# Optimization experiments

Measured on AMD Instinct MI355X. Metric: run time of the kernel, lower is better.

The kernel has to match this reference:

```python
import jax, jax.numpy as jnp
import numpy as np

N = 100000   # nodes
E = 800000   # edges (avg degree 8)
D = 128      # input_dim == output_dim
H = 4        # num_heads
DH = D // H  # head_dim = 32


def setup_inputs() -> dict:
    key = jax.random.key(0)
    ks = jax.random.split(key, 12)
    s = 1.0 / np.sqrt(D)
    x = jax.random.normal(ks[0], (N, D), jnp.float32)
    row = jnp.sort(jax.random.randint(ks[1], (E,), 0, N))  # destination (query) nodes
    col = jax.random.randint(ks[2], (E,), 0, N)            # source (key/value) nodes
    Wq = jax.random.normal(ks[3], (D, D), jnp.float32) * s
    bq = jax.random.normal(ks[4], (D,), jnp.float32) * 0.01
    Wk = jax.random.normal(ks[5], (D, D), jnp.float32) * s
    bk = jax.random.normal(ks[6], (D,), jnp.float32) * 0.01
    Wv = jax.random.normal(ks[7], (D, D), jnp.float32) * s
    bv = jax.random.normal(ks[8], (D,), jnp.float32) * 0.01
    Wo = jax.random.normal(ks[9], (D, D), jnp.float32) * s
    bo = jax.random.normal(ks[10], (D,), jnp.float32) * 0.01
    return {"x": x, "row": row, "col": col, "Wq": Wq, "bq": bq, "Wk": Wk,
            "bk": bk, "Wv": Wv, "bv": bv, "Wo": Wo, "bo": bo}


def reference(x, row, col, Wq, bq, Wk, bk, Wv, bv, Wo, bo):
    n = x.shape[0]
    # projections; reshape (N, head_dim, num_heads) exactly as the torch code
    # NOTE: source scales q by k.size(-1)**0.5 == sqrt(num_heads) (quirk, kept faithful)
    scale = jnp.asarray(H, x.dtype) ** 0.5
    q = ((x @ Wq.T + bq).reshape(n, DH, H)) / scale
    k = (x @ Wk.T + bk).reshape(n, DH, H)
    v = (x @ Wv.T + bv).reshape(n, DH, H)
    # bsddmm: per-edge, per-head scores s[e,h] = q[row[e],:,h] . k[col[e],:,h]
    s = jnp.einsum('edh,edh->eh', q[row], k[col])  # (E, H)
    # sparse row-wise softmax over incoming edges of each destination node
    m = jax.ops.segment_max(s, row, num_segments=n)      # (N, H)
    e = jnp.exp(s - m[row])                               # (E, H)
    z = jax.ops.segment_sum(e, row, num_segments=n)      # (N, H)
    a = e / z[row]                                        # (E, H) attention weights
    # bspmm: y[i,:,h] = sum_{e: row[e]=i} a[e,h] * v[col[e],:,h]
    y = jax.ops.segment_sum(a[:, None, :] * v[col], row, num_segments=n)  # (N, DH, H)
    return y.reshape(n, D) @ Wo.T + bo
```

## Files before the change

kernel.cpp:

```cpp
#include <hip/hip_runtime.h>
#include <hip/hip_bf16.h>
#include <hip/hip_fp16.h>
#include <math.h>

#define D 128
#define H 4

typedef __attribute__((ext_vector_type(8))) short bf16x8;
typedef __attribute__((ext_vector_type(4))) float f32x4;

__device__ __forceinline__ unsigned short f32_to_bf16_rne(float f) {
    union { float f; unsigned u; } c; c.f = f;
    unsigned u = c.u;
    return (unsigned short)((u + 0x7FFFu + ((u >> 16) & 1u)) >> 16);
}
__device__ __forceinline__ float bf16_to_f32(unsigned short h) {
    union { unsigned u; float f; } c; c.u = ((unsigned)h) << 16;
    return c.f;
}

__global__ __launch_bounds__(256) void convert_split(
    const float* __restrict__ in, unsigned short* __restrict__ hi,
    unsigned short* __restrict__ lo, int n4)
{
    int i = blockIdx.x * blockDim.x + threadIdx.x;
    if (i >= n4) return;
    float4 v = ((const float4*)in)[i];
    ushort4 h, l;
    h.x = f32_to_bf16_rne(v.x); l.x = f32_to_bf16_rne(v.x - bf16_to_f32(h.x));
    h.y = f32_to_bf16_rne(v.y); l.y = f32_to_bf16_rne(v.y - bf16_to_f32(h.y));
    h.z = f32_to_bf16_rne(v.z); l.z = f32_to_bf16_rne(v.z - bf16_to_f32(h.z));
    h.w = f32_to_bf16_rne(v.w); l.w = f32_to_bf16_rne(v.w - bf16_to_f32(h.w));
    ((ushort4*)hi)[i] = h;
    ((ushort4*)lo)[i] = l;
}

__global__ __launch_bounds__(256) void convert_w(
    const float* __restrict__ Wq, const float* __restrict__ Wk,
    const float* __restrict__ Wv, const float* __restrict__ Wo,
    unsigned short* __restrict__ wh, unsigned short* __restrict__ wl)
{
    int i = blockIdx.x * blockDim.x + threadIdx.x;
    if (i >= D * D) return;
    int r = i >> 7;
    int c = i & 127;
    int pr = ((r & 3) << 5) | (r >> 2);
    int pc = ((c & 3) << 5) | (c >> 2);
    const float* Ws[4] = {Wq, Wk, Wv, Wo};
#pragma unroll
    for (int m = 0; m < 4; ++m) {
        float f = Ws[m][i];
        unsigned short h = f32_to_bf16_rne(f);
        unsigned short l = f32_to_bf16_rne(f - bf16_to_f32(h));
        int dst = (m < 3) ? (pr * D + c) : (r * D + pc);
        wh[m * D * D + dst] = h;
        wl[m * D * D + dst] = l;
    }
}

#define RT 64

__global__ __launch_bounds__(512) void gemm_tile(
    const unsigned short* __restrict__ xh, const unsigned short* __restrict__ xl,
    const unsigned short* __restrict__ whAll, const unsigned short* __restrict__ wlAll,
    const float* __restrict__ b0, const float* __restrict__ b1,
    const float* __restrict__ b2,
    void* __restrict__ o0, void* __restrict__ o1, void* __restrict__ o2,
    float scale0, int n, int wbase, int halfmask, int permBias)
{
    __shared__ unsigned short Ah[RT * 128];
    __shared__ unsigned short Al[RT * 128];

    const int sel = blockIdx.y;
    const unsigned short* wh = whAll + (size_t)(wbase + sel) * D * D;
    const unsigned short* wl = wlAll + (size_t)(wbase + sel) * D * D;
    const float* bias = (sel == 0) ? b0 : (sel == 1 ? b1 : b2);
    void* out        = (sel == 0) ? o0 : (sel == 1 ? o1 : o2);
    const float scale = (sel == 0) ? scale0 : 1.0f;
    const bool halfOut = (halfmask >> sel) & 1;

    const int wid  = threadIdx.x >> 6;
    const int lane = threadIdx.x & 63;
    const int quad = lane >> 4;
    const int l16  = lane & 15;
    const int m0   = blockIdx.x * RT;

    const unsigned short* wrh = wh + (size_t)(wid * 16 + l16) * D + quad * 8;
    const unsigned short* wrl = wl + (size_t)(wid * 16 + l16) * D + quad * 8;
    bf16x8 bh[4], bl[4];
#pragma unroll
    for (int kc = 0; kc < 4; ++kc) {
        bh[kc] = *(const bf16x8*)(wrh + kc * 32);
        bl[kc] = *(const bf16x8*)(wrl + kc * 32);
    }

    for (int idx = threadIdx.x; idx < RT * 16; idx += 512) {
        int r  = idx >> 4;
        int c8 = idx & 15;
        int rg = m0 + r; if (rg > n - 1) rg = n - 1;
        int cs = ((c8 ^ (r & 15)) * 8);
        *(bf16x8*)&Ah[r * 128 + cs] = *(const bf16x8*)(xh + (size_t)rg * D + c8 * 8);
        *(bf16x8*)&Al[r * 128 + cs] = *(const bf16x8*)(xl + (size_t)rg * D + c8 * 8);
    }
    __syncthreads();

    f32x4 acc[4];
#pragma unroll
    for (int rt = 0; rt < 4; ++rt) acc[rt] = (f32x4){0.f, 0.f, 0.f, 0.f};

#pragma unroll
    for (int kc = 0; kc < 4; ++kc) {
        const int cs = ((quad + 4 * kc) ^ l16) * 8;
        bf16x8 ah[4], al[4];
#pragma unroll
        for (int rt = 0; rt < 4; ++rt) {
            const int r = rt * 16 + l16;
            ah[rt] = *(const bf16x8*)&Ah[r * 128 + cs];
            al[rt] = *(const bf16x8*)&Al[r * 128 + cs];
        }
#pragma unroll
        for (int rt = 0; rt < 4; ++rt)
            acc[rt] = __builtin_amdgcn_mfma_f32_16x16x32_bf16(ah[rt], bh[kc], acc[rt], 0, 0, 0);
#pragma unroll
        for (int rt = 0; rt < 4; ++rt)
            acc[rt] = __builtin_amdgcn_mfma_f32_16x16x32_bf16(al[rt], bh[kc], acc[rt], 0, 0, 0);
#pragma unroll
        for (int rt = 0; rt < 4; ++rt)
            acc[rt] = __builtin_amdgcn_mfma_f32_16x16x32_bf16(ah[rt], bl[kc], acc[rt], 0, 0, 0);
    }

    const int colg = wid * 16 + l16;
    const int bidx = permBias ? (((colg & 31) << 2) | (colg >> 5)) : colg;
    const float bv = bias[bidx];
    if (halfOut) {
        __half* oph = (__half*)out;
#pragma unroll
        for (int rt = 0; rt < 4; ++rt) {
#pragma unroll
            for (int r = 0; r < 4; ++r) {
                int rowg = m0 + rt * 16 + quad * 4 + r;
                if (rowg < n)
                    oph[(size_t)rowg * D + colg] = __float2half(acc[rt][r] + bv);
            }
        }
    } else {
        float* opf = (float*)out;
#pragma unroll
        for (int rt = 0; rt < 4; ++rt) {
#pragma unroll
            for (int r = 0; r < 4; ++r) {
                int rowg = m0 + rt * 16 + quad * 4 + r;
                if (rowg < n)
                    opf[(size_t)rowg * D + colg] = (acc[rt][r] + bv) * scale;
            }
        }
    }
}

__global__ void build_row_start(const int* __restrict__ row,
                                int* __restrict__ row_start, int n, int e)
{
    int i = blockIdx.x * blockDim.x + threadIdx.x;
    if (i > n) return;
    int lo = 0, hi = e;
    while (lo < hi) {
        int mid = (lo + hi) >> 1;
        if (row[mid] < i) lo = mid + 1; else hi = mid;
    }
    row_start[i] = lo;
}

#define MAXDEG 64
#define WPB 4

template<bool BIG>
__device__ __forceinline__ void edge_loop(
    int lane, int sub, int grp, int deg, int e0,
    const int* cmrow, const int* __restrict__ col,
    const float4 qa, const float4 qb,
    const __half* __restrict__ k, const __half* __restrict__ v,
    float& acc0, float& acc1, float& z)
{
    for (int e = 0; e < deg; e += 4) {
        const int ei = e + grp;
        int c0, c1, c2, c3, cs;
        if (!BIG) {
            const int4 cc = *(const int4*)&cmrow[e];
            c0 = cc.x; c1 = cc.y; c2 = cc.z; c3 = cc.w;
            cs = cmrow[ei < deg ? ei : deg - 1];
        } else {
            int es = ei < deg ? ei : deg - 1;
            cs = col[e0 + es];
            int e1 = e + 1 < deg ? e + 1 : deg - 1;
            int e2 = e + 2 < deg ? e + 2 : deg - 1;
            int e3 = e + 3 < deg ? e + 3 : deg - 1;
            c0 = col[e0 + e];
            c1 = col[e0 + e1];
            c2 = col[e0 + e2];
            c3 = col[e0 + e3];
        }
        __half2 v0 = ((const __half2*)(v + ((size_t)c0 << 7)))[lane];
        __half2 v1 = ((const __half2*)(v + ((size_t)c1 << 7)))[lane];
        __half2 v2 = ((const __half2*)(v + ((size_t)c2 << 7)))[lane];
        __half2 v3 = ((const __half2*)(v + ((size_t)c3 << 7)))[lane];
        union { bf16x8 v8; __half hx[8]; } ku;
        ku.v8 = *(const bf16x8*)(k + ((size_t)cs << 7) + sub * 8);
        float p = qa.x * __half2float(ku.hx[0]) + qa.y * __half2float(ku.hx[1])
                + qa.z * __half2float(ku.hx[2]) + qa.w * __half2float(ku.hx[3])
                + qb.x * __half2float(ku.hx[4]) + qb.y * __half2float(ku.hx[5])
                + qb.z * __half2float(ku.hx[6]) + qb.w * __half2float(ku.hx[7]);
        p += __shfl_xor(p, 1);
        p += __shfl_xor(p, 2);
        float ep = (ei < deg) ? __expf(p) : 0.f;
        float a0 = __shfl(ep,      4 * grp);
        float a1 = __shfl(ep, 16 + 4 * grp);
        float a2 = __shfl(ep, 32 + 4 * grp);
        float a3 = __shfl(ep, 48 + 4 * grp);
        z += (a0 + a1) + (a2 + a3);
        acc0 += a0 * __half2float(v0.x) + a1 * __half2float(v1.x)
              + a2 * __half2float(v2.x) + a3 * __half2float(v3.x);
        acc1 += a0 * __half2float(v0.y) + a1 * __half2float(v1.y)
              + a2 * __half2float(v2.y) + a3 * __half2float(v3.y);
    }
}

__global__ __launch_bounds__(WPB * 64) void edge_attn(
    const int* __restrict__ row_start,
    const float* __restrict__ q, const __half* __restrict__ k,
    const __half* __restrict__ v, const int* __restrict__ col,
    unsigned short* __restrict__ yh, unsigned short* __restrict__ yl, int n)
{
    __shared__ int cm[WPB][MAXDEG];

    const int wid  = threadIdx.x >> 6;
    const int lane = threadIdx.x & 63;
    const int node = blockIdx.x * WPB + wid;
    if (node >= n) return;

    const int e0  = row_start[node];
    const int deg = row_start[node + 1] - e0;
    const int sub = lane & 15;
    const int grp = lane >> 4;

    const float4* q4 = (const float4*)(q + (size_t)node * D) + sub * 2;
    const float4 qa = q4[0], qb = q4[1];

    float acc0 = 0.f, acc1 = 0.f, z = 0.f;

    if (deg <= MAXDEG) {
        const int dl4 = (deg + 3) & ~3;
        for (int i = lane; i < dl4; i += 64) {
            int ii = i < deg ? i : deg - 1;
            cm[wid][i] = col[e0 + ii];
        }
        edge_loop<false>(lane, sub, grp, deg, e0, cm[wid], col, qa, qb, k, v,
                         acc0, acc1, z);
    } else {
        edge_loop<true>(lane, sub, grp, deg, e0, cm[wid], col, qa, qb, k, v,
                        acc0, acc1, z);
    }

    const float rz = (z > 0.f) ? 1.f / z : 0.f;
    acc0 *= rz;
    acc1 *= rz;

    unsigned short h0 = f32_to_bf16_rne(acc0);
    unsigned short h1 = f32_to_bf16_rne(acc1);
    ushort2 hi2, lo2;
    hi2.x = h0; hi2.y = h1;
    lo2.x = f32_to_bf16_rne(acc0 - bf16_to_f32(h0));
    lo2.y = f32_to_bf16_rne(acc1 - bf16_to_f32(h1));
    ((ushort2*)yh)[(size_t)node * 64 + lane] = hi2;
    ((ushort2*)yl)[(size_t)node * 64 + lane] = lo2;
}

extern "C" void kernel_launch(void* const* d_in, const int* in_sizes, int n_in,
                              void* d_out, int out_size, void* d_ws, size_t ws_size,
                              hipStream_t stream)
{
    const float* x   = (const float*)d_in[0];
    const int*   row = (const int*)  d_in[1];
    const int*   col = (const int*)  d_in[2];
    const float* Wq  = (const float*)d_in[3];
    const float* bq  = (const float*)d_in[4];
    const float* Wk  = (const float*)d_in[5];
    const float* bk  = (const float*)d_in[6];
    const float* Wv  = (const float*)d_in[7];
    const float* bv  = (const float*)d_in[8];
    const float* Wo  = (const float*)d_in[9];
    const float* bo  = (const float*)d_in[10];
    float* out = (float*)d_out;

    const int n = in_sizes[0] / D;
    const int e = in_sizes[1];
    const size_t ND = (size_t)n * D;

    float* ws = (float*)d_ws;
    float*  q  = ws;
    __half* kh = (__half*)(ws + ND);
    __half* vh = kh + ND;
    unsigned short* xh = (unsigned short*)(ws + 2 * ND);
    unsigned short* xl = xh + ND;
    unsigned short* yh = xh;
    unsigned short* yl = xl;
    unsigned short* wh = (unsigned short*)(ws + 3 * ND);
    unsigned short* wl = wh + 4 * D * D;
    int* row_start = (int*)(wl + 4 * D * D);

    const int n4 = (int)(ND / 4);
    const int gx = (n + RT - 1) / RT;

    convert_w<<<(D * D + 255) / 256, 256, 0, stream>>>(Wq, Wk, Wv, Wo, wh, wl);
    convert_split<<<(n4 + 255) / 256, 256, 0, stream>>>(x, xh, xl, n4);

    gemm_tile<<<dim3(gx, 3), 512, 0, stream>>>(
        xh, xl, wh, wl, bq, bk, bv,
        (void*)q, (void*)kh, (void*)vh, 0.5f, n, 0, 6, 1);

    build_row_start<<<(n + 1 + 255) / 256, 256, 0, stream>>>(row, row_start, n, e);

    edge_attn<<<(n + WPB - 1) / WPB, WPB * 64, 0, stream>>>(
        row_start, q, kh, vh, col, yh, yl, n);

    gemm_tile<<<dim3(gx, 1), 512, 0, stream>>>(
        yh, yl, wh, wl, bo, bo, bo,
        (void*)out, (void*)out, (void*)out, 1.0f, n, 3, 0, 0);
}
```

Baseline: 293.2 us.

## Fuse fp32-to-bf16 split into GEMM and loop over Q/K/V in one block

Removes the separate convert_split kernel and has the GEMM read fp32 activations directly, splitting them into bf16 hi/lo in shared memory. The QKV GEMM now loads the x tile once and loops over the three weight matrices inside a block, instead of launching a 3-wide grid that re-reads x for each. edge_attn writes fp32 y, which the output GEMM converts on load. This saves an extra kernel launch and an intermediate hi/lo round trip through memory, but the grid has a third as many blocks and each block runs the three projections serially.

Result: slower. 308.1 us (+5.1%).

```diff
diff --git a/kernel.cpp b/kernel.cpp
--- a/kernel.cpp
+++ b/kernel.cpp
@@ -17,22 +17,6 @@
 __device__ __forceinline__ float bf16_to_f32(unsigned short h) {
     union { unsigned u; float f; } c; c.u = ((unsigned)h) << 16;
     return c.f;
-}
-
-__global__ __launch_bounds__(256) void convert_split(
-    const float* __restrict__ in, unsigned short* __restrict__ hi,
-    unsigned short* __restrict__ lo, int n4)
-{
-    int i = blockIdx.x * blockDim.x + threadIdx.x;
-    if (i >= n4) return;
-    float4 v = ((const float4*)in)[i];
-    ushort4 h, l;
-    h.x = f32_to_bf16_rne(v.x); l.x = f32_to_bf16_rne(v.x - bf16_to_f32(h.x));
-    h.y = f32_to_bf16_rne(v.y); l.y = f32_to_bf16_rne(v.y - bf16_to_f32(h.y));
-    h.z = f32_to_bf16_rne(v.z); l.z = f32_to_bf16_rne(v.z - bf16_to_f32(h.z));
-    h.w = f32_to_bf16_rne(v.w); l.w = f32_to_bf16_rne(v.w - bf16_to_f32(h.w));
-    ((ushort4*)hi)[i] = h;
-    ((ushort4*)lo)[i] = l;
 }
 
 __global__ __launch_bounds__(256) void convert_w(
@@ -60,8 +44,9 @@
 
 #define RT 64
 
-__global__ __launch_bounds__(512) void gemm_tile(
-    const unsigned short* __restrict__ xh, const unsigned short* __restrict__ xl,
+template<int NSEL>
+__global__ __launch_bounds__(512) void gemm_fused(
+    const float* __restrict__ A,
     const unsigned short* __restrict__ whAll, const unsigned short* __restrict__ wlAll,
     const float* __restrict__ b0, const float* __restrict__ b1,
     const float* __restrict__ b2,
@@ -71,87 +56,99 @@
     __shared__ unsigned short Ah[RT * 128];
     __shared__ unsigned short Al[RT * 128];
 
-    const int sel = blockIdx.y;
-    const unsigned short* wh = whAll + (size_t)(wbase + sel) * D * D;
-    const unsigned short* wl = wlAll + (size_t)(wbase + sel) * D * D;
-    const float* bias = (sel == 0) ? b0 : (sel == 1 ? b1 : b2);
-    void* out        = (sel == 0) ? o0 : (sel == 1 ? o1 : o2);
-    const float scale = (sel == 0) ? scale0 : 1.0f;
-    const bool halfOut = (halfmask >> sel) & 1;
-
     const int wid  = threadIdx.x >> 6;
     const int lane = threadIdx.x & 63;
     const int quad = lane >> 4;
     const int l16  = lane & 15;
     const int m0   = blockIdx.x * RT;
 
-    const unsigned short* wrh = wh + (size_t)(wid * 16 + l16) * D + quad * 8;
-    const unsigned short* wrl = wl + (size_t)(wid * 16 + l16) * D + quad * 8;
-    bf16x8 bh[4], bl[4];
-#pragma unroll
-    for (int kc = 0; kc < 4; ++kc) {
-        bh[kc] = *(const bf16x8*)(wrh + kc * 32);
-        bl[kc] = *(const bf16x8*)(wrl + kc * 32);
-    }
-
     for (int idx = threadIdx.x; idx < RT * 16; idx += 512) {
         int r  = idx >> 4;
         int c8 = idx & 15;
         int rg = m0 + r; if (rg > n - 1) rg = n - 1;
+        const float4* src = (const float4*)(A + (size_t)rg * D + c8 * 8);
+        float4 f0 = src[0], f1 = src[1];
+        float fa[8] = {f0.x, f0.y, f0.z, f0.w, f1.x, f1.y, f1.z, f1.w};
+        union { bf16x8 v; unsigned short s[8]; } hv, lv;
+#pragma unroll
+        for (int j = 0; j < 8; ++j) {
+            unsigned short hh = f32_to_bf16_rne(fa[j]);
+            hv.s[j] = hh;
+            lv.s[j] = f32_to_bf16_rne(fa[j] - bf16_to_f32(hh));
+        }
         int cs = ((c8 ^ (r & 15)) * 8);
-        *(bf16x8*)&Ah[r * 128 + cs] = *(const bf16x8*)(xh + (size_t)rg * D + c8 * 8);
-        *(bf16x8*)&Al[r * 128 + cs] = *(const bf16x8*)(xl + (size_t)rg * D + c8 * 8);
+        *(bf16x8*)&Ah[r * 128 + cs] = hv.v;
+        *(bf16x8*)&Al[r * 128 + cs] = lv.v;
     }
     __syncthreads();
 
-    f32x4 acc[4];
-#pragma unroll
-    for (int rt = 0; rt < 4; ++rt) acc[rt] = (f32x4){0.f, 0.f, 0.f, 0.f};
-
-#pragma unroll
-    for (int kc = 0; kc < 4; ++kc) {
-        const int cs = ((quad + 4 * kc) ^ l16) * 8;
-        bf16x8 ah[4], al[4];
-#pragma unroll
-        for (int rt = 0; rt < 4; ++rt) {
-            const int r = rt * 16 + l16;
-            ah[rt] = *(const bf16x8*)&Ah[r * 128 + cs];
-            al[rt] = *(const bf16x8*)&Al[r * 128 + cs];
-        }
-#pragma unroll
-        for (int rt = 0; rt < 4; ++rt)
-            acc[rt] = __builtin_amdgcn_mfma_f32_16x16x32_bf16(ah[rt], bh[kc], acc[rt], 0, 0, 0);
-#pragma unroll
-        for (int rt = 0; rt < 4; ++rt)
-            acc[rt] = __builtin_amdgcn_mfma_f32_16x16x32_bf16(al[rt], bh[kc], acc[rt], 0, 0, 0);
-#pragma unroll
-        for (int rt = 0; rt < 4; ++rt)
-            acc[rt] = __builtin_amdgcn_mfma_f32_16x16x32_bf16(ah[rt], bl[kc], acc[rt], 0, 0, 0);
-    }
-
-    const int colg = wid * 16 + l16;
-    const int bidx = permBias ? (((colg & 31) << 2) | (colg >> 5)) : colg;
-    const float bv = bias[bidx];
-    if (halfOut) {
-        __half* oph = (__half*)out;
-#pragma unroll
-        for (int rt = 0; rt < 4; ++rt) {
-#pragma unroll
-            for (int r = 0; r < 4; ++r) {
-                int rowg = m0 + rt * 16 + quad * 4 + r;
-                if (rowg < n)
-                    oph[(size_t)rowg * D + colg] = __float2half(acc[rt][r] + bv);
+#pragma unroll 1
+    for (int sel = 0; sel < NSEL; ++sel) {
+        const unsigned short* wh = whAll + (size_t)(wbase + sel) * D * D;
+        const unsigned short* wl = wlAll + (size_t)(wbase + sel) * D * D;
+        const float* bias = (sel == 0) ? b0 : (sel == 1 ? b1 : b2);
+        void* out        = (sel == 0) ? o0 : (sel == 1 ? o1 : o2);
+        const float scale = (sel == 0) ? scale0 : 1.0f;
+        const bool halfOut = (halfmask >> sel) & 1;
+
+        const unsigned short* wrh = wh + (size_t)(wid * 16 + l16) * D + quad * 8;
+        const unsigned short* wrl = wl + (size_t)(wid * 16 + l16) * D + quad * 8;
+        bf16x8 bh[4], bl[4];
+#pragma unroll
+        for (int kc = 0; kc < 4; ++kc) {
+            bh[kc] = *(const bf16x8*)(wrh + kc * 32);
+            bl[kc] = *(const bf16x8*)(wrl + kc * 32);
+        }
+
+        f32x4 acc[4];
+#pragma unroll
+        for (int rt = 0; rt < 4; ++rt) acc[rt] = (f32x4){0.f, 0.f, 0.f, 0.f};
+
+#pragma unroll
+        for (int kc = 0; kc < 4; ++kc) {
+            const int cs = ((quad + 4 * kc) ^ l16) * 8;
+            bf16x8 ah[4], al[4];
+#pragma unroll
+            for (int rt = 0; rt < 4; ++rt) {
+                const int r = rt * 16 + l16;
+                ah[rt] = *(const bf16x8*)&Ah[r * 128 + cs];
+                al[rt] = *(const bf16x8*)&Al[r * 128 + cs];
             }
-        }
-    } else {
-        float* opf = (float*)out;
-#pragma unroll
-        for (int rt = 0; rt < 4; ++rt) {
-#pragma unroll
-            for (int r = 0; r < 4; ++r) {
-                int rowg = m0 + rt * 16 + quad * 4 + r;
-                if (rowg < n)
-                    opf[(size_t)rowg * D + colg] = (acc[rt][r] + bv) * scale;
+#pragma unroll
+            for (int rt = 0; rt < 4; ++rt)
+                acc[rt] = __builtin_amdgcn_mfma_f32_16x16x32_bf16(ah[rt], bh[kc], acc[rt], 0, 0, 0);
+#pragma unroll
+            for (int rt = 0; rt < 4; ++rt)
+                acc[rt] = __builtin_amdgcn_mfma_f32_16x16x32_bf16(al[rt], bh[kc], acc[rt], 0, 0, 0);
+#pragma unroll
+            for (int rt = 0; rt < 4; ++rt)
+                acc[rt] = __builtin_amdgcn_mfma_f32_16x16x32_bf16(ah[rt], bl[kc], acc[rt], 0, 0, 0);
+        }
+
+        const int colg = wid * 16 + l16;
+        const int bidx = permBias ? (((colg & 31) << 2) | (colg >> 5)) : colg;
+        const float bv = bias[bidx];
+        if (halfOut) {
+            __half* oph = (__half*)out;
+#pragma unroll
+            for (int rt = 0; rt < 4; ++rt) {
+#pragma unroll
+                for (int r = 0; r < 4; ++r) {
+                    int rowg = m0 + rt * 16 + quad * 4 + r;
+                    if (rowg < n)
+                        oph[(size_t)rowg * D + colg] = __float2half(acc[rt][r] + bv);
+                }
+            }
+        } else {
+            float* opf = (float*)out;
+#pragma unroll
+            for (int rt = 0; rt < 4; ++rt) {
+#pragma unroll
+                for (int r = 0; r < 4; ++r) {
+                    int rowg = m0 + rt * 16 + quad * 4 + r;
+                    if (rowg < n)
+                        opf[(size_t)rowg * D + colg] = (acc[rt][r] + bv) * scale;
+                }
             }
         }
     }
@@ -228,7 +225,7 @@
     const int* __restrict__ row_start,
     const float* __restrict__ q, const __half* __restrict__ k,
     const __half* __restrict__ v, const int* __restrict__ col,
-    unsigned short* __restrict__ yh, unsigned short* __restrict__ yl, int n)
+    float* __restrict__ y, int n)
 {
     __shared__ int cm[WPB][MAXDEG];
 
@@ -264,14 +261,8 @@
     acc0 *= rz;
     acc1 *= rz;
 
-    unsigned short h0 = f32_to_bf16_rne(acc0);
-    unsigned short h1 = f32_to_bf16_rne(acc1);
-    ushort2 hi2, lo2;
-    hi2.x = h0; hi2.y = h1;
-    lo2.x = f32_to_bf16_rne(acc0 - bf16_to_f32(h0));
-    lo2.y = f32_to_bf16_rne(acc1 - bf16_to_f32(h1));
-    ((ushort2*)yh)[(size_t)node * 64 + lane] = hi2;
-    ((ushort2*)yl)[(size_t)node * 64 + lane] = lo2;
+    float2 o; o.x = acc0; o.y = acc1;
+    ((float2*)y)[(size_t)node * 64 + lane] = o;
 }
 
 extern "C" void kernel_launch(void* const* d_in, const int* in_sizes, int n_in,
@@ -299,30 +290,25 @@
     float*  q  = ws;
     __half* kh = (__half*)(ws + ND);
     __half* vh = kh + ND;
-    unsigned short* xh = (unsigned short*)(ws + 2 * ND);
-    unsigned short* xl = xh + ND;
-    unsigned short* yh = xh;
-    unsigned short* yl = xl;
+    float*  y  = ws + 2 * ND;
     unsigned short* wh = (unsigned short*)(ws + 3 * ND);
     unsigned short* wl = wh + 4 * D * D;
     int* row_start = (int*)(wl + 4 * D * D);
 
-    const int n4 = (int)(ND / 4);
     const int gx = (n + RT - 1) / RT;
 
     convert_w<<<(D * D + 255) / 256, 256, 0, stream>>>(Wq, Wk, Wv, Wo, wh, wl);
-    convert_split<<<(n4 + 255) / 256, 256, 0, stream>>>(x, xh, xl, n4);
-
-    gemm_tile<<<dim3(gx, 3), 512, 0, stream>>>(
-        xh, xl, wh, wl, bq, bk, bv,
+
+    gemm_fused<3><<<gx, 512, 0, stream>>>(
+        x, wh, wl, bq, bk, bv,
         (void*)q, (void*)kh, (void*)vh, 0.5f, n, 0, 6, 1);
 
     build_row_start<<<(n + 1 + 255) / 256, 256, 0, stream>>>(row, row_start, n, e);
 
     edge_attn<<<(n + WPB - 1) / WPB, WPB * 64, 0, stream>>>(
-        row_start, q, kh, vh, col, yh, yl, n);
-
-    gemm_tile<<<dim3(gx, 1), 512, 0, stream>>>(
-        yh, yl, wh, wl, bo, bo, bo,
+        row_start, q, kh, vh, col, y, n);
+
+    gemm_fused<1><<<gx, 512, 0, stream>>>(
+        y, wh, wl, bo, bo, bo,
         (void*)out, (void*)out, (void*)out, 1.0f, n, 3, 0, 0);
 }
```
